# Kernel tuning notes

Measured on AMD Instinct MI355X. Metric: run time of the kernel, lower is better.

Reference implementation:

```python
import jax, jax.numpy as jnp
import numpy as np
import math

T, B, Y = 512, 128, 22
H, R, L = 512, 512, 2
LOG_SQRT_2PI = 0.5 * math.log(2.0 * math.pi)


def _init(key, shape, fan_in):
    return (jax.random.normal(key, shape, dtype=jnp.float32) / np.sqrt(fan_in)).astype(jnp.float32)


def setup_inputs() -> dict:
    key = jax.random.key(0)
    ks = jax.random.split(key, 20)
    inp = {
        'states': jax.random.normal(ks[0], (T, B, Y), dtype=jnp.float32),
        # decoder MLP: Linear(R,H) -> ReLU -> Linear(H,H) -> ReLU
        'Wd1': _init(ks[1], (R, H), R), 'bd1': jnp.zeros((H,), jnp.float32),
        'Wd2': _init(ks[2], (H, H), H), 'bd2': jnp.zeros((H,), jnp.float32),
        # mean head and std head (Softplus)
        'Wm': _init(ks[3], (H, Y), H), 'bm': jnp.zeros((Y,), jnp.float32),
        'Ws': _init(ks[4], (H, Y), H), 'bs': jnp.zeros((Y,), jnp.float32),
        # GRU layer 0 (input Y) and layer 1 (input R); gates packed [r, z, n]
        'Wx0': _init(ks[5], (Y, 3 * R), Y), 'Wh0': _init(ks[6], (R, 3 * R), R),
        'bx0': jnp.zeros((3 * R,), jnp.float32), 'bh0': jnp.zeros((3 * R,), jnp.float32),
        'Wx1': _init(ks[7], (R, 3 * R), R), 'Wh1': _init(ks[8], (R, 3 * R), R),
        'bx1': jnp.zeros((3 * R,), jnp.float32), 'bh1': jnp.zeros((3 * R,), jnp.float32),
    }
    return inp


def _gru_cell(x, h, Wx, Wh, bx, bh):
    # PyTorch GRUCell math, gates packed as [r, z, n]
    gx = x @ Wx + bx              # [B, 3R]
    gh = h @ Wh + bh              # [B, 3R]
    xr, xz, xn = jnp.split(gx, 3, axis=-1)
    hr, hz, hn = jnp.split(gh, 3, axis=-1)
    r = jax.nn.sigmoid(xr + hr)
    z = jax.nn.sigmoid(xz + hz)
    n = jnp.tanh(xn + r * hn)
    return (1.0 - z) * n + z * h


def reference(states, Wd1, bd1, Wd2, bd2, Wm, bm, Ws, bs,
              Wx0, Wh0, bx0, bh0, Wx1, Wh1, bx1, bh1):
    h_init = jnp.zeros((L, B, R), dtype=states.dtype)

    def step(h, y_t):
        # decode from hidden BEFORE consuming y_t (as in the torch loop)
        dec = jax.nn.relu(jax.nn.relu(h[-1] @ Wd1 + bd1) @ Wd2 + bd2)
        mean = dec @ Wm + bm
        std = jax.nn.softplus(dec @ Ws + bs)
        nll_t = jnp.sum(0.5 * jnp.square((y_t - mean) / std) + jnp.log(std) + LOG_SQRT_2PI)
        h0 = _gru_cell(y_t, h[0], Wx0, Wh0, bx0, bh0)
        h1 = _gru_cell(h0, h[1], Wx1, Wh1, bx1, bh1)
        return jnp.stack([h0, h1]), nll_t

    _, nlls = jax.lax.scan(step, h_init, states)
    return jnp.sum(nlls)
```

## Files before the change

### kernel.cpp

```cpp
#include <hip/hip_runtime.h>
#include <math.h>

#define T_ 512
#define B_ 128
#define Y_ 22
#define NWG 256
#define NSLOT (T_ + 3)
#define LOG_SQRT_2PI 0.91893853320467274178f

typedef float f32x4 __attribute__((ext_vector_type(4)));
typedef short bf16x8 __attribute__((ext_vector_type(8)));

#define MFMA(a, b, c) __builtin_amdgcn_mfma_f32_16x16x32_bf16(a, b, c, 0, 0, 0)

#define OFF_WH0 0UL
#define SZ_GATE (32UL * 3 * 64 * 128 * 2)
#define OFF_WX0 (OFF_WH0 + SZ_GATE)
#define SZ_WX0 (32UL * 3 * 4 * 128 * 2)
#define OFF_WX1 (OFF_WX0 + SZ_WX0)
#define OFF_WH1 (OFF_WX1 + SZ_GATE)
#define OFF_WD1 (OFF_WH1 + SZ_GATE)
#define SZ_SQ (32UL * 64 * 128 * 2)
#define OFF_WD2 (OFF_WD1 + SZ_SQ)
#define OFF_WM (OFF_WD2 + SZ_SQ)
#define SZ_HD (2UL * 64 * 128 * 2)
#define OFF_WS2 (OFF_WM + SZ_HD)
#define OFF_YBF (OFF_WS2 + SZ_HD)
#define SZ_YBF (512UL * 128 * 32 * 2)
#define OFF_H0B (OFF_YBF + SZ_YBF)
#define SZ_HB (2UL * 128 * 512 * 2)
#define OFF_H1B (OFF_H0B + SZ_HB)
#define OFF_D1 (OFF_H1B + SZ_HB)
#define OFF_D2 (OFF_D1 + SZ_HB)
#define OFF_NLL (OFF_D2 + SZ_HB)
#define OFF_ROOT (OFF_NLL + 64)
#define OFF_SUB (OFF_ROOT + 64UL * NSLOT)
#define OFF_END (OFF_SUB + 16UL * 2176)

#define SMEM_BYTES 106496

struct Params {
  const float* states;
  const float *Wd1, *bd1, *Wd2, *bd2, *Wm, *bm, *Ws, *bs;
  const float *Wx0, *Wh0, *bx0, *bh0, *Wx1, *Wh1, *bx1, *bh1;
  char* ws;
  float* out;
};

__device__ __forceinline__ unsigned short f2bf(float f) {
  unsigned x = __float_as_uint(f);
  return (unsigned short)((x + 0x7fffu + ((x >> 16) & 1u)) >> 16);
}

__device__ __forceinline__ unsigned cpoll(const unsigned* p) {
  unsigned r;
  asm volatile("global_load_dword %0, %1, off sc0 sc1\n\ts_waitcnt vmcnt(0)"
               : "=v"(r)
               : "v"(p)
               : "memory");
  return r;
}
__device__ __forceinline__ bf16x8 cload16(const void* p) {
  bf16x8 r;
  asm volatile("global_load_dwordx4 %0, %1, off sc0 sc1" : "=v"(r) : "v"(p));
  return r;
}
__device__ __forceinline__ void cstore2(void* p, unsigned short v) {
  unsigned vv = v;
  asm volatile("global_store_short %0, %1, off sc0 sc1" ::"v"(p), "v"(vv) : "memory");
}
__device__ __forceinline__ void vwait0() {
  asm volatile("s_waitcnt vmcnt(0)" ::: "memory");
  __builtin_amdgcn_sched_barrier(0);
}

__device__ void prep_gate(const float* src, unsigned short* d, size_t t0, size_t nt) {
  const size_t n = 32UL * 3 * 64 * 128;
  for (size_t i = t0; i < n; i += nt) {
    int e = (int)(i & 7), cl = (int)((i >> 3) & 15), k8 = (int)((i >> 7) & 63);
    int g = (int)((i >> 13) % 3), cg = (int)(i / 24576);
    int k = k8 * 8 + e, nn = g * 512 + cg * 16 + cl;
    d[i] = f2bf(src[(size_t)k * 1536 + nn]);
  }
}
__device__ void prep_sq(const float* src, unsigned short* d, size_t t0, size_t nt) {
  const size_t n = 32UL * 64 * 128;
  for (size_t i = t0; i < n; i += nt) {
    int e = (int)(i & 7), cl = (int)((i >> 3) & 15), k8 = (int)((i >> 7) & 63);
    int cg = (int)(i >> 13);
    int k = k8 * 8 + e, nn = cg * 16 + cl;
    d[i] = f2bf(src[(size_t)k * 512 + nn]);
  }
}
__device__ void prep_head(const float* src, unsigned short* d, size_t t0, size_t nt) {
  const size_t n = 2UL * 64 * 128;
  for (size_t i = t0; i < n; i += nt) {
    int e = (int)(i & 7), cl = (int)((i >> 3) & 15), k8 = (int)((i >> 7) & 63);
    int hc = (int)(i >> 13);
    int k = k8 * 8 + e, nn = hc * 16 + cl;
    d[i] = (nn < Y_) ? f2bf(src[(size_t)k * Y_ + nn]) : (unsigned short)0;
  }
}

extern "C" __global__ void rnn_prep(Params p) {
  char* ws = p.ws;
  size_t t0 = (size_t)blockIdx.x * blockDim.x + threadIdx.x;
  size_t nt = (size_t)gridDim.x * blockDim.x;
  {
    unsigned* z = (unsigned*)(ws + OFF_H0B);
    size_t n = (OFF_END - OFF_H0B) / 4;
    for (size_t i = t0; i < n; i += nt) z[i] = 0u;
  }
  {
    unsigned short* yb = (unsigned short*)(ws + OFF_YBF);
    size_t n = (size_t)T_ * B_ * 32;
    for (size_t i = t0; i < n; i += nt) {
      int k = (int)(i & 31);
      size_t tb = i >> 5;
      float v = (k < Y_) ? p.states[tb * Y_ + k] : 0.f;
      yb[i] = f2bf(v);
    }
  }
  prep_gate(p.Wh0, (unsigned short*)(ws + OFF_WH0), t0, nt);
  prep_gate(p.Wx1, (unsigned short*)(ws + OFF_WX1), t0, nt);
  prep_gate(p.Wh1, (unsigned short*)(ws + OFF_WH1), t0, nt);
  {
    unsigned short* d = (unsigned short*)(ws + OFF_WX0);
    size_t n = 32UL * 3 * 4 * 128;
    for (size_t i = t0; i < n; i += nt) {
      int e = (int)(i & 7), cl = (int)((i >> 3) & 15), k8 = (int)((i >> 7) & 3);
      int g = (int)((i >> 9) % 3), cg = (int)(i / 1536);
      int k = k8 * 8 + e, nn = g * 512 + cg * 16 + cl;
      d[i] = (k < Y_) ? f2bf(p.Wx0[(size_t)k * 1536 + nn]) : (unsigned short)0;
    }
  }
  prep_sq(p.Wd1, (unsigned short*)(ws + OFF_WD1), t0, nt);
  prep_sq(p.Wd2, (unsigned short*)(ws + OFF_WD2), t0, nt);
  prep_head(p.Wm, (unsigned short*)(ws + OFF_WM), t0, nt);
  prep_head(p.Ws, (unsigned short*)(ws + OFF_WS2), t0, nt);
}

__device__ __forceinline__ void ldscpy(char* dst, const char* src, int bytes) {
  f32x4* d = (f32x4*)dst;
  const f32x4* s = (const f32x4*)src;
  int n = bytes >> 4;
  for (int i = threadIdx.x; i < n; i += 256) d[i] = s[i];
}

__device__ __forceinline__ void gbar(char* ws, int s, int bid) {
  __syncthreads();
  if (threadIdx.x == 0) {
    unsigned* sc = (unsigned*)(ws + OFF_SUB) + (size_t)(bid & 15) * 544 + s;
    unsigned* root = (unsigned*)(ws + OFF_ROOT) + (size_t)s * 16;
    atomicAdd(sc, 1u);
    if (bid < 16) {
      while (cpoll(sc) < 16u) __builtin_amdgcn_s_sleep(1);
      atomicAdd(root, 1u);
    }
    while (cpoll(root) < 16u) __builtin_amdgcn_s_sleep(1);
  }
  __syncthreads();
}

extern "C" __global__ void __launch_bounds__(256) rnn_main(Params p) {
  extern __shared__ char smem[];
  char* ws = p.ws;
  unsigned short* h0b = (unsigned short*)(ws + OFF_H0B);
  unsigned short* h1b = (unsigned short*)(ws + OFF_H1B);
  unsigned short* d1b = (unsigned short*)(ws + OFF_D1);
  unsigned short* d2b = (unsigned short*)(ws + OFF_D2);
  const unsigned short* ybf = (const unsigned short*)(ws + OFF_YBF);

  const int bid = blockIdx.x, tid = threadIdx.x;
  const int wv = tid >> 6, lane = tid & 63;
  const int l16 = lane & 15, lq = lane >> 4;

  if (bid < 128) {
    int cg = bid & 31;
    ldscpy(smem, ws + OFF_WX1 + (size_t)cg * 49152, 49152);
    ldscpy(smem + 49152, ws + OFF_WH1 + (size_t)cg * 49152, 49152);
  } else if (bid < 192) {
    int cg = (bid - 128) & 31;
    ldscpy(smem, ws + OFF_WH0 + (size_t)cg * 49152, 49152);
    ldscpy(smem + 49152, ws + OFF_WX0 + (size_t)cg * 3072, 3072);
  } else if (bid < 224) {
    int cg = bid - 192;
    ldscpy(smem, ws + OFF_WD1 + (size_t)cg * 16384, 16384);
    if (cg < 8) {
      int hc = cg & 1;
      ldscpy(smem + 16384, ws + OFF_WM + (size_t)hc * 16384, 16384);
      ldscpy(smem + 32768, ws + OFF_WS2 + (size_t)hc * 16384, 16384);
    }
  } else {
    int cg = bid - 224;
    ldscpy(smem, ws + OFF_WD2 + (size_t)cg * 16384, 16384);
  }

  f32x4 hreg = {0.f, 0.f, 0.f, 0.f};
  float cA = 0.f, cB = 0.f, cC = 0.f, cD = 0.f, cM = 0.f, cS = 0.f;
  if (bid < 128) {
    const int cg = bid & 31, kh = wv & 1;
    const int j = cg * 16 + l16;
    if (kh == 0) {
      cA = p.bx1[j] + p.bh1[j];
      cB = p.bx1[512 + j] + p.bh1[512 + j];
      cC = p.bx1[1024 + j];
      cD = p.bh1[1024 + j];
    }
  } else if (bid < 192) {
    const int cg = (bid - 128) & 31;
    const int j = cg * 16 + l16;
    cA = p.bx0[j] + p.bh0[j];
    cB = p.bx0[512 + j] + p.bh0[512 + j];
    cC = p.bx0[1024 + j];
    cD = p.bh0[1024 + j];
  } else if (bid < 224) {
    const int cg = bid - 192;
    cA = p.bd1[cg * 16 + l16];
    if (cg < 8 && wv < 2) {
      const int col = (cg & 1) * 16 + l16;
      cM = (col < Y_) ? p.bm[col] : 0.f;
      cS = (col < Y_) ? p.bs[col] : 0.f;
    }
  } else {
    cA = p.bd2[(bid - 224) * 16 + l16];
  }
  __syncthreads();

  for (int s = 0; s < NSLOT; ++s) {
    if (bid < 128) {
      const int ms = bid >> 5;
      const int mt = wv >> 1, kh = wv & 1;
      float* part = (float*)(smem + 98304);
      const bool act = (s >= 1 && s <= T_);
      const int m0 = 32 * ms + 16 * mt;
      const int j = (bid & 31) * 16 + l16;
      f32x4 aR = {0.f, 0.f, 0.f, 0.f}, aZ = aR, aXN = aR, aHN = aR;
      if (act) {
        const unsigned short* A1 = h0b + ((s - 1) & 1) * 65536;
        const unsigned short* A2 = h1b + ((s - 2) & 1) * 65536;
        const int ab = (m0 + l16) * 512 + kh * 256 + 8 * lq;
        bf16x8 a1[8], a2[8];
#pragma unroll
        for (int kk = 0; kk < 8; ++kk) {
          a1[kk] = cload16(A1 + ab + kk * 32);
          a2[kk] = cload16(A2 + ab + kk * 32);
        }
        if (kh == 0) {
          aR = f32x4{cA, cA, cA, cA};
          aZ = f32x4{cB, cB, cB, cB};
          aXN = f32x4{cC, cC, cC, cC};
          aHN = f32x4{cD, cD, cD, cD};
        }
        const unsigned short* wx = (const unsigned short*)smem;
        const unsigned short* wh = wx + 24576;
        vwait0();
#pragma unroll
        for (int kk = 0; kk < 8; ++kk) {
          int bo = ((kh * 8 + kk) * 4 + lq) * 128 + l16 * 8;
          aR = MFMA(a1[kk], *(const bf16x8*)(wx + bo), aR);
          aZ = MFMA(a1[kk], *(const bf16x8*)(wx + 8192 + bo), aZ);
          aXN = MFMA(a1[kk], *(const bf16x8*)(wx + 16384 + bo), aXN);
          aR = MFMA(a2[kk], *(const bf16x8*)(wh + bo), aR);
          aZ = MFMA(a2[kk], *(const bf16x8*)(wh + 8192 + bo), aZ);
          aHN = MFMA(a2[kk], *(const bf16x8*)(wh + 16384 + bo), aHN);
        }
        if (kh == 1) {
          float* q = part + (mt * 64 + lane) * 16;
          *(f32x4*)(q + 0) = aR;
          *(f32x4*)(q + 4) = aZ;
          *(f32x4*)(q + 8) = aXN;
          *(f32x4*)(q + 12) = aHN;
        }
      }
      __syncthreads();
      if (act && kh == 0) {
        const float* q = part + (mt * 64 + lane) * 16;
        aR += *(const f32x4*)(q + 0);
        aZ += *(const f32x4*)(q + 4);
        aXN += *(const f32x4*)(q + 8);
        aHN += *(const f32x4*)(q + 12);
        unsigned short* hbn = h1b + ((s - 1) & 1) * 65536;
#pragma unroll
        for (int i = 0; i < 4; ++i) {
          int row = m0 + lq * 4 + i;
          float r = 1.f / (1.f + __expf(-aR[i]));
          float z = 1.f / (1.f + __expf(-aZ[i]));
          float n = tanhf(aXN[i] + r * aHN[i]);
          float hv = (1.f - z) * n + z * hreg[i];
          hreg[i] = hv;
          cstore2(hbn + row * 512 + j, f2bf(hv));
        }
      }
    } else if (bid < 192) {
      const int idx = bid - 128, ms = idx >> 5, cg = idx & 31;
      if (s < T_) {
        const unsigned short* A = h0b + ((s - 1) & 1) * 65536;
        const int m0 = 64 * ms + 16 * wv;
        const int j = cg * 16 + l16;
        const int ab = (m0 + l16) * 512 + 8 * lq;
        bf16x8 a[16];
#pragma unroll
        for (int kk = 0; kk < 16; ++kk) a[kk] = cload16(A + ab + kk * 32);
        const unsigned short* wh = (const unsigned short*)smem;
        const unsigned short* wx = wh + 24576;
        f32x4 aR = {cA, cA, cA, cA}, aZ = {cB, cB, cB, cB};
        f32x4 aN = {cC, cC, cC, cC}, aH = {cD, cD, cD, cD};
        {
          bf16x8 ya = *(const bf16x8*)(ybf + (size_t)s * (128 * 32) + (m0 + l16) * 32 + 8 * lq);
          int bo = lq * 128 + l16 * 8;
          aR = MFMA(ya, *(const bf16x8*)(wx + bo), aR);
          aZ = MFMA(ya, *(const bf16x8*)(wx + 512 + bo), aZ);
          aN = MFMA(ya, *(const bf16x8*)(wx + 1024 + bo), aN);
        }
        vwait0();
#pragma unroll
        for (int kk = 0; kk < 16; ++kk) {
          int bo = (kk * 4 + lq) * 128 + l16 * 8;
          aR = MFMA(a[kk], *(const bf16x8*)(wh + bo), aR);
          aZ = MFMA(a[kk], *(const bf16x8*)(wh + 8192 + bo), aZ);
          aH = MFMA(a[kk], *(const bf16x8*)(wh + 16384 + bo), aH);
        }
        unsigned short* hbn = h0b + (s & 1) * 65536;
#pragma unroll
        for (int i = 0; i < 4; ++i) {
          int row = m0 + lq * 4 + i;
          float r = 1.f / (1.f + __expf(-aR[i]));
          float z = 1.f / (1.f + __expf(-aZ[i]));
          float n = tanhf(aN[i] + r * aH[i]);
          float hv = (1.f - z) * n + z * hreg[i];
          hreg[i] = hv;
          cstore2(hbn + row * 512 + j, f2bf(hv));
        }
      }
    } else if (bid < 224) {
      const int cg = bid - 192;
      const bool actH = (cg < 8 && wv < 2 && s >= 3);
      bf16x8 hd[16];
      int m0h = 0;
      if (actH) {
        const unsigned short* Ah = d2b + ((s - 3) & 1) * 65536;
        m0h = 32 * (cg >> 1) + 16 * wv;
        const int abh = (m0h + l16) * 512 + 8 * lq;
#pragma unroll
        for (int kk = 0; kk < 16; ++kk) hd[kk] = cload16(Ah + abh + kk * 32);
      }
      if (s >= 1 && s <= T_) {
        const unsigned short* A = h1b + ((s - 2) & 1) * 65536;
        unsigned short* dst = d1b + ((s - 1) & 1) * 65536;
        const unsigned short* wd = (const unsigned short*)smem;
        const int j = cg * 16 + l16;
#pragma unroll
        for (int half = 0; half < 2; ++half) {
          int m0 = (wv * 2 + half) * 16;
          int ab = (m0 + l16) * 512 + 8 * lq;
          bf16x8 a[16];
#pragma unroll
          for (int kk = 0; kk < 16; ++kk) a[kk] = cload16(A + ab + kk * 32);
          f32x4 acc = {cA, cA, cA, cA};
          vwait0();
#pragma unroll
          for (int kk = 0; kk < 16; ++kk) {
            int bo = (kk * 4 + lq) * 128 + l16 * 8;
            acc = MFMA(a[kk], *(const bf16x8*)(wd + bo), acc);
          }
#pragma unroll
          for (int i = 0; i < 4; ++i) {
            int row = m0 + lq * 4 + i;
            float v = acc[i];
            cstore2(dst + row * 512 + j, f2bf(v > 0.f ? v : 0.f));
          }
        }
      }
      if (actH) {
        const int tau = s - 3;
        const int hc = cg & 1;
        const unsigned short* wm = (const unsigned short*)(smem + 16384);
        const unsigned short* wst = (const unsigned short*)(smem + 32768);
        const int col = hc * 16 + l16;
        f32x4 aM = {cM, cM, cM, cM}, aS = {cS, cS, cS, cS};
        vwait0();
#pragma unroll
        for (int kk = 0; kk < 16; ++kk) {
          int bo = (kk * 4 + lq) * 128 + l16 * 8;
          aM = MFMA(hd[kk], *(const bf16x8*)(wm + bo), aM);
          aS = MFMA(hd[kk], *(const bf16x8*)(wst + bo), aS);
        }
        float lsum = 0.f;
        if (col < Y_) {
#pragma unroll
          for (int i = 0; i < 4; ++i) {
            int row = m0h + lq * 4 + i;
            float sp = aS[i];
            float sd = (sp > 20.f) ? sp : log1pf(__expf(sp));
            float yv = p.states[((size_t)tau * B_ + row) * Y_ + col];
            float tt = (yv - aM[i]) / sd;
            lsum += 0.5f * tt * tt + __logf(sd) + LOG_SQRT_2PI;
          }
        }
#pragma unroll
        for (int off = 32; off > 0; off >>= 1) lsum += __shfl_down(lsum, off);
        if (lane == 0) atomicAdd((float*)(ws + OFF_NLL), lsum);
      }
    } else {
      const int cg = bid - 224;
      if (s >= 2 && s <= T_ + 1) {
        const unsigned short* A = d1b + ((s - 2) & 1) * 65536;
        unsigned short* dst = d2b + ((s - 2) & 1) * 65536;
        const unsigned short* wd = (const unsigned short*)smem;
        const int j = cg * 16 + l16;
#pragma unroll
        for (int half = 0; half < 2; ++half) {
          int m0 = (wv * 2 + half) * 16;
          int ab = (m0 + l16) * 512 + 8 * lq;
          bf16x8 a[16];
#pragma unroll
          for (int kk = 0; kk < 16; ++kk) a[kk] = cload16(A + ab + kk * 32);
          f32x4 acc = {cA, cA, cA, cA};
          vwait0();
#pragma unroll
          for (int kk = 0; kk < 16; ++kk) {
            int bo = (kk * 4 + lq) * 128 + l16 * 8;
            acc = MFMA(a[kk], *(const bf16x8*)(wd + bo), acc);
          }
#pragma unroll
          for (int i = 0; i < 4; ++i) {
            int row = m0 + lq * 4 + i;
            float v = acc[i];
            cstore2(dst + row * 512 + j, f2bf(v > 0.f ? v : 0.f));
          }
        }
      }
    }
    gbar(ws, s, bid);
  }

  if (bid == 0 && tid == 0) {
    unsigned u = cpoll((const unsigned*)(ws + OFF_NLL));
    p.out[0] = __uint_as_float(u);
  }
}

extern "C" void kernel_launch(void* const* d_in, const int* in_sizes, int n_in,
                              void* d_out, int out_size, void* d_ws, size_t ws_size,
                              hipStream_t stream) {
  if (ws_size < OFF_END) return;
  Params p;
  p.states = (const float*)d_in[0];
  p.Wd1 = (const float*)d_in[1];
  p.bd1 = (const float*)d_in[2];
  p.Wd2 = (const float*)d_in[3];
  p.bd2 = (const float*)d_in[4];
  p.Wm = (const float*)d_in[5];
  p.bm = (const float*)d_in[6];
  p.Ws = (const float*)d_in[7];
  p.bs = (const float*)d_in[8];
  p.Wx0 = (const float*)d_in[9];
  p.Wh0 = (const float*)d_in[10];
  p.bx0 = (const float*)d_in[11];
  p.bh0 = (const float*)d_in[12];
  p.Wx1 = (const float*)d_in[13];
  p.Wh1 = (const float*)d_in[14];
  p.bx1 = (const float*)d_in[15];
  p.bh1 = (const float*)d_in[16];
  p.ws = (char*)d_ws;
  p.out = (float*)d_out;

  hipLaunchKernelGGL(rnn_prep, dim3(512), dim3(256), 0, stream, p);

  hipFuncSetAttribute((const void*)rnn_main, hipFuncAttributeMaxDynamicSharedMemorySize,
                      SMEM_BYTES);
  void* args[] = {&p};
  hipError_t rc = hipLaunchCooperativeKernel((const void*)rnn_main, dim3(NWG), dim3(256),
                                             args, SMEM_BYTES, stream);
  if (rc != hipSuccess) {
    hipLaunchKernelGGL(rnn_main, dim3(NWG), dim3(256), SMEM_BYTES, stream, p);
  }
}
```

Before: 5.382 ms.

## Replace tree grid barrier with flag array, drop split-K reduction in GRU1

Replaces the two-level atomic counter grid barrier with a per-slot flag array that each block sets and that a whole wavefront polls with vector loads. This is meant to cut barrier latency on the serial per-timestep critical path. The GRU layer-1 blocks now have two waves each doing the full K dimension, rather than four waves splitting K and reducing through LDS. That removes an LDS round-trip and a __syncthreads, but leaves half the waves idle and doubles the per-wave MFMA chain. The decoder blocks also issue the first half's loads early, alongside the head loads, so their latency overlaps.

Measured after the change: 6.312 ms. 1.17x slower.

```diff
diff --git a/kernel.cpp b/kernel.cpp
--- a/kernel.cpp
+++ b/kernel.cpp
@@ -10,6 +10,7 @@
 
 typedef float f32x4 __attribute__((ext_vector_type(4)));
 typedef short bf16x8 __attribute__((ext_vector_type(8)));
+typedef int i32x4 __attribute__((ext_vector_type(4)));
 
 #define MFMA(a, b, c) __builtin_amdgcn_mfma_f32_16x16x32_bf16(a, b, c, 0, 0, 0)
 
@@ -33,11 +34,10 @@
 #define OFF_D1 (OFF_H1B + SZ_HB)
 #define OFF_D2 (OFF_D1 + SZ_HB)
 #define OFF_NLL (OFF_D2 + SZ_HB)
-#define OFF_ROOT (OFF_NLL + 64)
-#define OFF_SUB (OFF_ROOT + 64UL * NSLOT)
-#define OFF_END (OFF_SUB + 16UL * 2176)
-
-#define SMEM_BYTES 106496
+#define OFF_FLAG (OFF_NLL + 64)
+#define OFF_END (OFF_FLAG + 4UL * 256 * NSLOT)
+
+#define SMEM_BYTES 98304
 
 struct Params {
   const float* states;
@@ -55,6 +55,14 @@
 __device__ __forceinline__ unsigned cpoll(const unsigned* p) {
   unsigned r;
   asm volatile("global_load_dword %0, %1, off sc0 sc1\n\ts_waitcnt vmcnt(0)"
+               : "=v"(r)
+               : "v"(p)
+               : "memory");
+  return r;
+}
+__device__ __forceinline__ i32x4 cpoll4(const void* p) {
+  i32x4 r;
+  asm volatile("global_load_dwordx4 %0, %1, off sc0 sc1\n\ts_waitcnt vmcnt(0)"
                : "=v"(r)
                : "v"(p)
                : "memory");
@@ -149,15 +157,16 @@
 
 __device__ __forceinline__ void gbar(char* ws, int s, int bid) {
   __syncthreads();
-  if (threadIdx.x == 0) {
-    unsigned* sc = (unsigned*)(ws + OFF_SUB) + (size_t)(bid & 15) * 544 + s;
-    unsigned* root = (unsigned*)(ws + OFF_ROOT) + (size_t)s * 16;
-    atomicAdd(sc, 1u);
-    if (bid < 16) {
-      while (cpoll(sc) < 16u) __builtin_amdgcn_s_sleep(1);
-      atomicAdd(root, 1u);
-    }
-    while (cpoll(root) < 16u) __builtin_amdgcn_s_sleep(1);
+  if (threadIdx.x < 64) {
+    unsigned* flags = (unsigned*)(ws + OFF_FLAG) + (size_t)s * 256;
+    if (threadIdx.x == 0) atomicExch(flags + bid, 1u);
+    const i32x4* fp = (const i32x4*)flags + threadIdx.x;
+    for (;;) {
+      i32x4 v = cpoll4(fp);
+      bool ok = (v.x == 1) & (v.y == 1) & (v.z == 1) & (v.w == 1);
+      if (__all(ok)) break;
+      __builtin_amdgcn_s_sleep(1);
+    }
   }
   __syncthreads();
 }
@@ -199,9 +208,9 @@
   f32x4 hreg = {0.f, 0.f, 0.f, 0.f};
   float cA = 0.f, cB = 0.f, cC = 0.f, cD = 0.f, cM = 0.f, cS = 0.f;
   if (bid < 128) {
-    const int cg = bid & 31, kh = wv & 1;
+    const int cg = bid & 31;
     const int j = cg * 16 + l16;
-    if (kh == 0) {
+    if (wv < 2) {
       cA = p.bx1[j] + p.bh1[j];
       cB = p.bx1[512 + j] + p.bh1[512 + j];
       cC = p.bx1[1024 + j];
@@ -230,34 +239,26 @@
   for (int s = 0; s < NSLOT; ++s) {
     if (bid < 128) {
       const int ms = bid >> 5;
-      const int mt = wv >> 1, kh = wv & 1;
-      float* part = (float*)(smem + 98304);
-      const bool act = (s >= 1 && s <= T_);
-      const int m0 = 32 * ms + 16 * mt;
-      const int j = (bid & 31) * 16 + l16;
-      f32x4 aR = {0.f, 0.f, 0.f, 0.f}, aZ = aR, aXN = aR, aHN = aR;
-      if (act) {
+      if (wv < 2 && s >= 1 && s <= T_) {
+        const int m0 = 32 * ms + 16 * wv;
+        const int j = (bid & 31) * 16 + l16;
         const unsigned short* A1 = h0b + ((s - 1) & 1) * 65536;
         const unsigned short* A2 = h1b + ((s - 2) & 1) * 65536;
-        const int ab = (m0 + l16) * 512 + kh * 256 + 8 * lq;
-        bf16x8 a1[8], a2[8];
-#pragma unroll
-        for (int kk = 0; kk < 8; ++kk) {
+        const int ab = (m0 + l16) * 512 + 8 * lq;
+        bf16x8 a1[16], a2[16];
+#pragma unroll
+        for (int kk = 0; kk < 16; ++kk) {
           a1[kk] = cload16(A1 + ab + kk * 32);
           a2[kk] = cload16(A2 + ab + kk * 32);
         }
-        if (kh == 0) {
-          aR = f32x4{cA, cA, cA, cA};
-          aZ = f32x4{cB, cB, cB, cB};
-          aXN = f32x4{cC, cC, cC, cC};
-          aHN = f32x4{cD, cD, cD, cD};
-        }
         const unsigned short* wx = (const unsigned short*)smem;
         const unsigned short* wh = wx + 24576;
+        f32x4 aR = {cA, cA, cA, cA}, aZ = {cB, cB, cB, cB};
+        f32x4 aXN = {cC, cC, cC, cC}, aHN = {cD, cD, cD, cD};
         vwait0();
 #pragma unroll
-        for (int kk = 0; kk < 8; ++kk) {
-          int bo = ((kh * 8 + kk) * 4 + lq) * 128 + l16 * 8;
+        for (int kk = 0; kk < 16; ++kk) {
+          int bo = (kk * 4 + lq) * 128 + l16 * 8;
           aR = MFMA(a1[kk], *(const bf16x8*)(wx + bo), aR);
           aZ = MFMA(a1[kk], *(const bf16x8*)(wx + 8192 + bo), aZ);
           aXN = MFMA(a1[kk], *(const bf16x8*)(wx + 16384 + bo), aXN);
@@ -265,21 +266,6 @@
           aZ = MFMA(a2[kk], *(const bf16x8*)(wh + 8192 + bo), aZ);
           aHN = MFMA(a2[kk], *(const bf16x8*)(wh + 16384 + bo), aHN);
         }
-        if (kh == 1) {
-          float* q = part + (mt * 64 + lane) * 16;
-          *(f32x4*)(q + 0) = aR;
-          *(f32x4*)(q + 4) = aZ;
-          *(f32x4*)(q + 8) = aXN;
-          *(f32x4*)(q + 12) = aHN;
-        }
-      }
-      __syncthreads();
-      if (act && kh == 0) {
-        const float* q = part + (mt * 64 + lane) * 16;
-        aR += *(const f32x4*)(q + 0);
-        aZ += *(const f32x4*)(q + 4);
-        aXN += *(const f32x4*)(q + 8);
-        aHN += *(const f32x4*)(q + 12);
         unsigned short* hbn = h1b + ((s - 1) & 1) * 65536;
 #pragma unroll
         for (int i = 0; i < 4; ++i) {
@@ -336,8 +322,11 @@
     } else if (bid < 224) {
       const int cg = bid - 192;
       const bool actH = (cg < 8 && wv < 2 && s >= 3);
-      bf16x8 hd[16];
+      const bool actD = (s >= 1 && s <= T_);
+      bf16x8 hd[16], a0[16];
       int m0h = 0;
+      const unsigned short* A = h1b + ((s - 2) & 1) * 65536;
+      const int j = cg * 16 + l16;
       if (actH) {
         const unsigned short* Ah = d2b + ((s - 3) & 1) * 65536;
         m0h = 32 * (cg >> 1) + 16 * wv;
@@ -345,15 +334,34 @@
 #pragma unroll
         for (int kk = 0; kk < 16; ++kk) hd[kk] = cload16(Ah + abh + kk * 32);
       }
-      if (s >= 1 && s <= T_) {
-        const unsigned short* A = h1b + ((s - 2) & 1) * 65536;
+      if (actD) {
+        const int m0 = (wv * 2) * 16;
+        const int ab = (m0 + l16) * 512 + 8 * lq;
+#pragma unroll
+        for (int kk = 0; kk < 16; ++kk) a0[kk] = cload16(A + ab + kk * 32);
+      }
+      if (actD) {
         unsigned short* dst = d1b + ((s - 1) & 1) * 65536;
         const unsigned short* wd = (const unsigned short*)smem;
-        const int j = cg * 16 + l16;
-#pragma unroll
-        for (int half = 0; half < 2; ++half) {
-          int m0 = (wv * 2 + half) * 16;
-          int ab = (m0 + l16) * 512 + 8 * lq;
+        {
+          const int m0 = (wv * 2) * 16;
+          f32x4 acc = {cA, cA, cA, cA};
+          vwait0();
+#pragma unroll
+          for (int kk = 0; kk < 16; ++kk) {
+            int bo = (kk * 4 + lq) * 128 + l16 * 8;
+            acc = MFMA(a0[kk], *(const bf16x8*)(wd + bo), acc);
+          }
+#pragma unroll
+          for (int i = 0; i < 4; ++i) {
+            int row = m0 + lq * 4 + i;
+            float v = acc[i];
+            cstore2(dst + row * 512 + j, f2bf(v > 0.f ? v : 0.f));
+          }
+        }
+        {
+          const int m0 = (wv * 2 + 1) * 16;
+          const int ab = (m0 + l16) * 512 + 8 * lq;
           bf16x8 a[16];
 #pragma unroll
           for (int kk = 0; kk < 16; ++kk) a[kk] = cload16(A + ab + kk * 32);
@@ -379,7 +387,7 @@
         const unsigned short* wst = (const unsigned short*)(smem + 32768);
         const int col = hc * 16 + l16;
         f32x4 aM = {cM, cM, cM, cM}, aS = {cS, cS, cS, cS};
-        vwait0();
+        if (!actD) vwait0();
 #pragma unroll
         for (int kk = 0; kk < 16; ++kk) {
           int bo = (kk * 4 + lq) * 128 + l16 * 8;
```
